# Optimization experiments

Hardware: AMD Instinct MI355X
Metric: run time of the kernel (lower is better)

## Reference

```python
import jax, jax.numpy as jnp
import numpy as np

B, S, DK = 32, 2048, 64

def setup_inputs() -> dict:
    key = jax.random.key(0)
    kq, kk, kv = jax.random.split(key, 3)
    Q = jax.random.normal(kq, (B, S, DK), dtype=jnp.float32)
    K = jax.random.normal(kk, (B, S, DK), dtype=jnp.float32)
    V = jax.random.normal(kv, (B, S, DK), dtype=jnp.float32)
    return {"Q": Q, "K": K, "V": V}

def reference(Q, K, V):
    # attn_scores = Q K^T / sqrt(d_k); full [B,S,S] probs materialized (naive, non-flash)
    d_k = Q.shape[-1]
    scores = jnp.einsum('bqd,bkd->bqk', Q, K) / jnp.sqrt(jnp.asarray(d_k, Q.dtype))
    probs = jax.nn.softmax(scores, axis=-1)
    return jnp.einsum('bqk,bkd->bqd', probs, V)
```

## Files before the change

kernel.cpp:

```cpp
#include <hip/hip_runtime.h>
#include <hip/hip_bf16.h>

#define BATCH 32
#define SEQ   2048
#define DKK   64

constexpr int QT  = 128;
constexpr int KT  = 64;
constexpr int NW  = 4;
constexpr int NIT = SEQ / KT;
constexpr int LST = 66;

typedef __attribute__((ext_vector_type(8)))  short bf16x8;
typedef __attribute__((ext_vector_type(16))) float f32x16;

__device__ __forceinline__ unsigned cvt2(float a, float b) {
    union { __hip_bfloat162 h; unsigned u; } c;
    c.h = __float22bfloat162_rn(make_float2(a, b));
    return c.u;
}

__device__ __forceinline__ float fast_exp2(float x) {
#if __has_builtin(__builtin_amdgcn_exp2f)
    return __builtin_amdgcn_exp2f(x);
#else
    return exp2f(x);
#endif
}

__global__ __launch_bounds__(256, 2) void attn_fwd(
        const float* __restrict__ Q, const float* __restrict__ K,
        const float* __restrict__ V, float* __restrict__ O) {
    __shared__ short Kb[2][KT][LST];
    __shared__ short Vt[2][DKK][LST];
    __shared__ short Pb[NW][32][LST];

    const int tid  = threadIdx.x;
    const int w    = tid >> 6;
    const int lane = tid & 63;
    const int hi   = lane >> 5;
    const int l31  = lane & 31;
    const int b    = blockIdx.y;
    const int q0   = blockIdx.x * QT + w * 32;

    const float qscale = 0.125f * 1.44269504088896340736f;
    bf16x8 qfrag[4];
    #pragma unroll
    for (int c = 0; c < 4; ++c) {
        const float* qp = Q + ((size_t)b * SEQ + q0 + l31) * DKK + 16*c + 8*hi;
        float4 a  = *(const float4*)qp;
        float4 a2 = *(const float4*)(qp + 4);
        union { bf16x8 v; unsigned u[4]; } f;
        f.u[0] = cvt2(a.x*qscale,  a.y*qscale);
        f.u[1] = cvt2(a.z*qscale,  a.w*qscale);
        f.u[2] = cvt2(a2.x*qscale, a2.y*qscale);
        f.u[3] = cvt2(a2.z*qscale, a2.w*qscale);
        qfrag[c] = f.v;
    }

    f32x16 o0 = {}, o1 = {};
    float lsum = 0.f;

    const float* Kbase = K + (size_t)b * SEQ * DKK;
    const float* Vbase = V + (size_t)b * SEQ * DKK;

    const int krow0 = tid >> 4;
    const int kcol  = (tid & 15) << 2;
    const int vd    = tid & 63;
    const int vg    = (tid >> 6) << 4;

    float4 kp[4];
    float  vp[16];
    auto load_regs = [&](int t) {
        const float* Kg = Kbase + (size_t)(t * KT) * DKK;
        #pragma unroll
        for (int i = 0; i < 4; ++i)
            kp[i] = *(const float4*)(Kg + (size_t)(krow0 + 16*i) * DKK + kcol);
        const float* Vg = Vbase + (size_t)(t * KT + vg) * DKK + vd;
        #pragma unroll
        for (int i = 0; i < 16; ++i) vp[i] = Vg[(size_t)i * DKK];
    };
    auto write_lds = [&](int buf) {
        #pragma unroll
        for (int i = 0; i < 4; ++i) {
            int2 kk;
            kk.x = (int)cvt2(kp[i].x, kp[i].y);
            kk.y = (int)cvt2(kp[i].z, kp[i].w);
            *(int2*)&Kb[buf][krow0 + 16*i][kcol] = kk;
        }
        union { bf16x8 v; unsigned u[4]; } t0, t1;
        t0.u[0] = cvt2(vp[0],  vp[1]);  t0.u[1] = cvt2(vp[2],  vp[3]);
        t0.u[2] = cvt2(vp[4],  vp[5]);  t0.u[3] = cvt2(vp[6],  vp[7]);
        t1.u[0] = cvt2(vp[8],  vp[9]);  t1.u[1] = cvt2(vp[10], vp[11]);
        t1.u[2] = cvt2(vp[12], vp[13]); t1.u[3] = cvt2(vp[14], vp[15]);
        *(bf16x8*)&Vt[buf][vd][vg]     = t0.v;
        *(bf16x8*)&Vt[buf][vd][vg + 8] = t1.v;
    };

    load_regs(0);
    write_lds(0);
    load_regs(1);
    __syncthreads();

    for (int it = 0; it < NIT; ++it) {
        const int cur = it & 1;

        #pragma unroll
        for (int kt2 = 0; kt2 < 2; ++kt2) {
            f32x16 acc = {};
            #pragma unroll
            for (int c = 0; c < 4; ++c) {
                bf16x8 kf = *(const bf16x8*)&Kb[cur][32*kt2 + l31][16*c + 8*hi];
                acc = __builtin_amdgcn_mfma_f32_32x32x16_bf16(kf, qfrag[c], acc, 0, 0, 0);
            }
            float p[16];
            #pragma unroll
            for (int r = 0; r < 16; ++r) { p[r] = fast_exp2(acc[r]); lsum += p[r]; }
            #pragma unroll
            for (int G = 0; G < 4; ++G) {
                int2 pw;
                pw.x = (int)cvt2(p[4*G],     p[4*G + 1]);
                pw.y = (int)cvt2(p[4*G + 2], p[4*G + 3]);
                *(int2*)&Pb[w][l31][32*kt2 + 8*G + 4*hi] = pw;
            }
        }

        #pragma unroll
        for (int c = 0; c < 4; ++c) {
            bf16x8 pf  = *(const bf16x8*)&Pb[w][l31][16*c + 8*hi];
            bf16x8 vf0 = *(const bf16x8*)&Vt[cur][l31     ][16*c + 8*hi];
            bf16x8 vf1 = *(const bf16x8*)&Vt[cur][32 + l31][16*c + 8*hi];
            o0 = __builtin_amdgcn_mfma_f32_32x32x16_bf16(vf0, pf, o0, 0, 0, 0);
            o1 = __builtin_amdgcn_mfma_f32_32x32x16_bf16(vf1, pf, o1, 0, 0, 0);
        }

        if (it + 1 < NIT) {
            write_lds(1 - cur);
            if (it + 2 < NIT) load_regs(it + 2);
            __syncthreads();
        }
    }

    float s = lsum;
    s += __shfl_xor(s, 32);
    const float inv = 1.0f / s;

    float* op = O + ((size_t)b * SEQ + q0 + l31) * DKK;
    #pragma unroll
    for (int G = 0; G < 4; ++G) {
        float4 st;
        st.x = o0[4*G + 0] * inv; st.y = o0[4*G + 1] * inv;
        st.z = o0[4*G + 2] * inv; st.w = o0[4*G + 3] * inv;
        *(float4*)(op + 8*G + 4*hi) = st;
        st.x = o1[4*G + 0] * inv; st.y = o1[4*G + 1] * inv;
        st.z = o1[4*G + 2] * inv; st.w = o1[4*G + 3] * inv;
        *(float4*)(op + 32 + 8*G + 4*hi) = st;
    }
}

extern "C" void kernel_launch(void* const* d_in, const int* in_sizes, int n_in,
                              void* d_out, int out_size, void* d_ws, size_t ws_size,
                              hipStream_t stream) {
    const float* Q = (const float*)d_in[0];
    const float* K = (const float*)d_in[1];
    const float* V = (const float*)d_in[2];
    float* O = (float*)d_out;
    dim3 grid(SEQ / QT, BATCH);
    attn_fwd<<<grid, dim3(256), 0, stream>>>(Q, K, V, O);
}
```

Before: 142.0 us.

## Pass P fragments via cross-lane shuffles instead of LDS, halve query tile

The softmax probabilities are no longer written to and reread from shared memory. Each lane packs its bf16 P values in registers and swaps halves with its partner lane via __shfl_xor, building the MFMA B operand directly. The query tile shrinks from 128 to 64 rows (2 waves per block), so each thread loads twice as much K/V per tile. This doubles the grid and frees LDS, but K/V reuse per block is halved and per-thread register pressure from the staging loads rises.

```diff
diff --git a/kernel.cpp b/kernel.cpp
--- a/kernel.cpp
+++ b/kernel.cpp
@@ -5,9 +5,8 @@
 #define SEQ   2048
 #define DKK   64
 
-constexpr int QT  = 128;
+constexpr int QT  = 64;
 constexpr int KT  = 64;
-constexpr int NW  = 4;
 constexpr int NIT = SEQ / KT;
 constexpr int LST = 66;
 
@@ -28,12 +27,11 @@
 #endif
 }
 
-__global__ __launch_bounds__(256, 2) void attn_fwd(
+__global__ __launch_bounds__(128, 2) void attn_fwd(
         const float* __restrict__ Q, const float* __restrict__ K,
         const float* __restrict__ V, float* __restrict__ O) {
     __shared__ short Kb[2][KT][LST];
     __shared__ short Vt[2][DKK][LST];
-    __shared__ short Pb[NW][32][LST];
 
     const int tid  = threadIdx.x;
     const int w    = tid >> 6;
@@ -67,34 +65,36 @@
     const int krow0 = tid >> 4;
     const int kcol  = (tid & 15) << 2;
     const int vd    = tid & 63;
-    const int vg    = (tid >> 6) << 4;
+    const int vg    = (tid >> 6) << 5;
 
-    float4 kp[4];
-    float  vp[16];
+    float4 kp[8];
+    float  vp[32];
     auto load_regs = [&](int t) {
         const float* Kg = Kbase + (size_t)(t * KT) * DKK;
         #pragma unroll
-        for (int i = 0; i < 4; ++i)
-            kp[i] = *(const float4*)(Kg + (size_t)(krow0 + 16*i) * DKK + kcol);
+        for (int i = 0; i < 8; ++i)
+            kp[i] = *(const float4*)(Kg + (size_t)(krow0 + 8*i) * DKK + kcol);
         const float* Vg = Vbase + (size_t)(t * KT + vg) * DKK + vd;
         #pragma unroll
-        for (int i = 0; i < 16; ++i) vp[i] = Vg[(size_t)i * DKK];
+        for (int i = 0; i < 32; ++i) vp[i] = Vg[(size_t)i * DKK];
     };
     auto write_lds = [&](int buf) {
         #pragma unroll
-        for (int i = 0; i < 4; ++i) {
+        for (int i = 0; i < 8; ++i) {
             int2 kk;
             kk.x = (int)cvt2(kp[i].x, kp[i].y);
             kk.y = (int)cvt2(kp[i].z, kp[i].w);
-            *(int2*)&Kb[buf][krow0 + 16*i][kcol] = kk;
+            *(int2*)&Kb[buf][krow0 + 8*i][kcol] = kk;
         }
-        union { bf16x8 v; unsigned u[4]; } t0, t1;
-        t0.u[0] = cvt2(vp[0],  vp[1]);  t0.u[1] = cvt2(vp[2],  vp[3]);
-        t0.u[2] = cvt2(vp[4],  vp[5]);  t0.u[3] = cvt2(vp[6],  vp[7]);
-        t1.u[0] = cvt2(vp[8],  vp[9]);  t1.u[1] = cvt2(vp[10], vp[11]);
-        t1.u[2] = cvt2(vp[12], vp[13]); t1.u[3] = cvt2(vp[14], vp[15]);
-        *(bf16x8*)&Vt[buf][vd][vg]     = t0.v;
-        *(bf16x8*)&Vt[buf][vd][vg + 8] = t1.v;
+        #pragma unroll
+        for (int j = 0; j < 4; ++j) {
+            union { bf16x8 v; unsigned u[4]; } t;
+            t.u[0] = cvt2(vp[8*j + 0], vp[8*j + 1]);
+            t.u[1] = cvt2(vp[8*j + 2], vp[8*j + 3]);
+            t.u[2] = cvt2(vp[8*j + 4], vp[8*j + 5]);
+            t.u[3] = cvt2(vp[8*j + 6], vp[8*j + 7]);
+            *(bf16x8*)&Vt[buf][vd][vg + 8*j] = t.v;
+        }
     };
 
     load_regs(0);
@@ -105,6 +105,7 @@
     for (int it = 0; it < NIT; ++it) {
         const int cur = it & 1;
 
+        unsigned pA[2][4], pB[2][4];
         #pragma unroll
         for (int kt2 = 0; kt2 < 2; ++kt2) {
             f32x16 acc = {};
@@ -113,25 +114,36 @@
                 bf16x8 kf = *(const bf16x8*)&Kb[cur][32*kt2 + l31][16*c + 8*hi];
                 acc = __builtin_amdgcn_mfma_f32_32x32x16_bf16(kf, qfrag[c], acc, 0, 0, 0);
             }
-            float p[16];
-            #pragma unroll
-            for (int r = 0; r < 16; ++r) { p[r] = fast_exp2(acc[r]); lsum += p[r]; }
             #pragma unroll
             for (int G = 0; G < 4; ++G) {
-                int2 pw;
-                pw.x = (int)cvt2(p[4*G],     p[4*G + 1]);
-                pw.y = (int)cvt2(p[4*G + 2], p[4*G + 3]);
-                *(int2*)&Pb[w][l31][32*kt2 + 8*G + 4*hi] = pw;
+                float p0 = fast_exp2(acc[4*G + 0]);
+                float p1 = fast_exp2(acc[4*G + 1]);
+                float p2 = fast_exp2(acc[4*G + 2]);
+                float p3 = fast_exp2(acc[4*G + 3]);
+                lsum += (p0 + p1) + (p2 + p3);
+                pA[kt2][G] = cvt2(p0, p1);
+                pB[kt2][G] = cvt2(p2, p3);
             }
         }
 
         #pragma unroll
         for (int c = 0; c < 4; ++c) {
-            bf16x8 pf  = *(const bf16x8*)&Pb[w][l31][16*c + 8*hi];
+            const int kk2 = c >> 1, cc = c & 1;
+            unsigned a0 = pA[kk2][2*cc], a1 = pA[kk2][2*cc + 1];
+            unsigned b0 = pB[kk2][2*cc], b1 = pB[kk2][2*cc + 1];
+            unsigned locA = hi ? a1 : a0, sndA = hi ? a0 : a1;
+            unsigned locB = hi ? b1 : b0, sndB = hi ? b0 : b1;
+            unsigned remA = (unsigned)__shfl_xor((int)sndA, 32);
+            unsigned remB = (unsigned)__shfl_xor((int)sndB, 32);
+            union { bf16x8 v; unsigned u[4]; } pf;
+            pf.u[0] = hi ? remA : locA;
+            pf.u[1] = hi ? remB : locB;
+            pf.u[2] = hi ? locA : remA;
+            pf.u[3] = hi ? locB : remB;
             bf16x8 vf0 = *(const bf16x8*)&Vt[cur][l31     ][16*c + 8*hi];
             bf16x8 vf1 = *(const bf16x8*)&Vt[cur][32 + l31][16*c + 8*hi];
-            o0 = __builtin_amdgcn_mfma_f32_32x32x16_bf16(vf0, pf, o0, 0, 0, 0);
-            o1 = __builtin_amdgcn_mfma_f32_32x32x16_bf16(vf1, pf, o1, 0, 0, 0);
+            o0 = __builtin_amdgcn_mfma_f32_32x32x16_bf16(vf0, pf.v, o0, 0, 0, 0);
+            o1 = __builtin_amdgcn_mfma_f32_32x32x16_bf16(vf1, pf.v, o1, 0, 0, 0);
         }
 
         if (it + 1 < NIT) {
@@ -166,5 +178,5 @@
     const float* V = (const float*)d_in[2];
     float* O = (float*)d_out;
     dim3 grid(SEQ / QT, BATCH);
-    attn_fwd<<<grid, dim3(256), 0, stream>>>(Q, K, V, O);
+    attn_fwd<<<grid, dim3(128), 0, stream>>>(Q, K, V, O);
 }
```

Result: slower. 154.0 us (+8.5%).

## Split the key dimension in two and combine partial outputs in a second kernel

Applied to the files above, without the earlier changes.

Adds split-K (flash-decoding style) parallelism. Each block handles half the key sequence and writes unnormalised fp16 partial outputs plus partial row sums to workspace, and a combine kernel sums and normalises them. The base grid is 16x32=512 blocks of 256 threads, so doubling to 1024 blocks is meant to fill the 256 CUs of the GPU better. In exchange it adds a second launch, extra global traffic for the partials, and fp16 rounding of the partial outputs. Because no running max is subtracted, unnormalised sums held in fp16 could overflow for large scores, and the path falls back to the single kernel if the workspace is too small.

```diff
diff --git a/kernel.cpp b/kernel.cpp
--- a/kernel.cpp
+++ b/kernel.cpp
@@ -8,11 +8,11 @@
 constexpr int QT  = 128;
 constexpr int KT  = 64;
 constexpr int NW  = 4;
-constexpr int NIT = SEQ / KT;
 constexpr int LST = 66;
 
 typedef __attribute__((ext_vector_type(8)))  short bf16x8;
 typedef __attribute__((ext_vector_type(16))) float f32x16;
+typedef __attribute__((ext_vector_type(2)))  __fp16 h2v;
 
 __device__ __forceinline__ unsigned cvt2(float a, float b) {
     union { __hip_bfloat162 h; unsigned u; } c;
@@ -28,9 +28,12 @@
 #endif
 }
 
-__global__ __launch_bounds__(256, 2) void attn_fwd(
+template<int SPLIT>
+__global__ __launch_bounds__(256, 2) void attn_main(
         const float* __restrict__ Q, const float* __restrict__ K,
-        const float* __restrict__ V, float* __restrict__ O) {
+        const float* __restrict__ V, float* __restrict__ O,
+        __fp16* __restrict__ Opart, float* __restrict__ Lpart) {
+    constexpr int NIT = SEQ / SPLIT / KT;
     __shared__ short Kb[2][KT][LST];
     __shared__ short Vt[2][DKK][LST];
     __shared__ short Pb[NW][32][LST];
@@ -41,6 +44,7 @@
     const int hi   = lane >> 5;
     const int l31  = lane & 31;
     const int b    = blockIdx.y;
+    const int ks   = blockIdx.z;
     const int q0   = blockIdx.x * QT + w * 32;
 
     const float qscale = 0.125f * 1.44269504088896340736f;
@@ -61,8 +65,8 @@
     f32x16 o0 = {}, o1 = {};
     float lsum = 0.f;
 
-    const float* Kbase = K + (size_t)b * SEQ * DKK;
-    const float* Vbase = V + (size_t)b * SEQ * DKK;
+    const float* Kbase = K + ((size_t)b * SEQ + (size_t)ks * (SEQ / SPLIT)) * DKK;
+    const float* Vbase = V + ((size_t)b * SEQ + (size_t)ks * (SEQ / SPLIT)) * DKK;
 
     const int krow0 = tid >> 4;
     const int kcol  = (tid & 15) << 2;
@@ -143,19 +147,55 @@
 
     float s = lsum;
     s += __shfl_xor(s, 32);
-    const float inv = 1.0f / s;
-
-    float* op = O + ((size_t)b * SEQ + q0 + l31) * DKK;
-    #pragma unroll
-    for (int G = 0; G < 4; ++G) {
-        float4 st;
-        st.x = o0[4*G + 0] * inv; st.y = o0[4*G + 1] * inv;
-        st.z = o0[4*G + 2] * inv; st.w = o0[4*G + 3] * inv;
-        *(float4*)(op + 8*G + 4*hi) = st;
-        st.x = o1[4*G + 0] * inv; st.y = o1[4*G + 1] * inv;
-        st.z = o1[4*G + 2] * inv; st.w = o1[4*G + 3] * inv;
-        *(float4*)(op + 32 + 8*G + 4*hi) = st;
-    }
+
+    const size_t row = (size_t)b * SEQ + q0 + l31;
+    if constexpr (SPLIT == 1) {
+        const float inv = 1.0f / s;
+        float* op = O + row * DKK;
+        #pragma unroll
+        for (int G = 0; G < 4; ++G) {
+            float4 st;
+            st.x = o0[4*G + 0] * inv; st.y = o0[4*G + 1] * inv;
+            st.z = o0[4*G + 2] * inv; st.w = o0[4*G + 3] * inv;
+            *(float4*)(op + 8*G + 4*hi) = st;
+            st.x = o1[4*G + 0] * inv; st.y = o1[4*G + 1] * inv;
+            st.z = o1[4*G + 2] * inv; st.w = o1[4*G + 3] * inv;
+            *(float4*)(op + 32 + 8*G + 4*hi) = st;
+        }
+    } else {
+        __fp16* wp = Opart + ((size_t)ks * BATCH * SEQ + row) * DKK;
+        #pragma unroll
+        for (int G = 0; G < 4; ++G) {
+            union { h2v h[2]; uint2 u; } t;
+            t.h[0] = __builtin_amdgcn_cvt_pkrtz(o0[4*G + 0], o0[4*G + 1]);
+            t.h[1] = __builtin_amdgcn_cvt_pkrtz(o0[4*G + 2], o0[4*G + 3]);
+            *(uint2*)(wp + 8*G + 4*hi) = t.u;
+            t.h[0] = __builtin_amdgcn_cvt_pkrtz(o1[4*G + 0], o1[4*G + 1]);
+            t.h[1] = __builtin_amdgcn_cvt_pkrtz(o1[4*G + 2], o1[4*G + 3]);
+            *(uint2*)(wp + 32 + 8*G + 4*hi) = t.u;
+        }
+        if (hi == 0) Lpart[(size_t)ks * BATCH * SEQ + row] = s;
+    }
+}
+
+__global__ __launch_bounds__(256) void attn_combine(
+        const __fp16* __restrict__ Opart, const float* __restrict__ Lpart,
+        float* __restrict__ O) {
+    const int gid    = blockIdx.x * 256 + threadIdx.x;
+    const int rowIdx = gid >> 4;
+    const int d4     = (gid & 15) << 2;
+    const size_t NROW = (size_t)BATCH * SEQ;
+    const __fp16* p0 = Opart + (size_t)rowIdx * DKK + d4;
+    const __fp16* p1 = Opart + (NROW + rowIdx) * DKK + d4;
+    const float inv = 1.0f / (Lpart[rowIdx] + Lpart[NROW + rowIdx]);
+    h2v a0 = *(const h2v*)p0, a1 = *(const h2v*)(p0 + 2);
+    h2v b0 = *(const h2v*)p1, b1 = *(const h2v*)(p1 + 2);
+    float4 st;
+    st.x = ((float)a0[0] + (float)b0[0]) * inv;
+    st.y = ((float)a0[1] + (float)b0[1]) * inv;
+    st.z = ((float)a1[0] + (float)b1[0]) * inv;
+    st.w = ((float)a1[1] + (float)b1[1]) * inv;
+    *(float4*)(O + (size_t)rowIdx * DKK + d4) = st;
 }
 
 extern "C" void kernel_launch(void* const* d_in, const int* in_sizes, int n_in,
@@ -165,6 +205,19 @@
     const float* K = (const float*)d_in[1];
     const float* V = (const float*)d_in[2];
     float* O = (float*)d_out;
-    dim3 grid(SEQ / QT, BATCH);
-    attn_fwd<<<grid, dim3(256), 0, stream>>>(Q, K, V, O);
-}
+
+    constexpr size_t OPART_BYTES = (size_t)2 * BATCH * SEQ * DKK * 2;
+    constexpr size_t LPART_BYTES = (size_t)2 * BATCH * SEQ * 4;
+    constexpr size_t NEED = OPART_BYTES + LPART_BYTES;
+
+    if (ws_size >= NEED) {
+        __fp16* Opart = (__fp16*)d_ws;
+        float*  Lpart = (float*)((char*)d_ws + OPART_BYTES);
+        dim3 grid(SEQ / QT, BATCH, 2);
+        attn_main<2><<<grid, dim3(256), 0, stream>>>(Q, K, V, O, Opart, Lpart);
+        attn_combine<<<(BATCH * SEQ * 16) / 256, dim3(256), 0, stream>>>(Opart, Lpart, O);
+    } else {
+        dim3 grid(SEQ / QT, BATCH, 1);
+        attn_main<1><<<grid, dim3(256), 0, stream>>>(Q, K, V, O, nullptr, nullptr);
+    }
+}
```

After: 154.0 us. 1.08x slower.
